# Kernel tuning notes

Measured on AMD Instinct MI355X. Metric: run time of the kernel, lower is better.

## Reference

```python
import jax, jax.numpy as jnp
import numpy as np

N = 100000      # nodes
E = 1600000     # edges (avg degree 16)
IN, HID, OUT = 128, 64, 64


def setup_inputs() -> dict:
    key = jax.random.key(0)
    ks = jax.random.split(key, 8)
    s = 0.05
    return {
        "x": jax.random.normal(ks[0], (N, IN), jnp.float32),
        "edge_index": jax.random.randint(ks[1], (2, E), 0, N, dtype=jnp.int32),
        "W1": jax.random.normal(ks[2], (IN, HID), jnp.float32) * s,
        "b1": jnp.zeros((HID,), jnp.float32),
        "W2": jax.random.normal(ks[3], (HID, HID), jnp.float32) * s,
        "b2": jnp.zeros((HID,), jnp.float32),
        "W3": jax.random.normal(ks[4], (HID, OUT), jnp.float32) * s,
        "b3": jnp.zeros((OUT,), jnp.float32),
    }


def reference(x, edge_index, W1, b1, W2, b2, W3, b3):
    src, dst = edge_index[0], edge_index[1]

    def gcn_conv(h, W, b):
        # GCNConv(normalize=False): dense linear, gather source features,
        # scatter-add into target nodes, add bias.
        m = (h @ W)[src]                                   # [E, F_out]
        return jax.ops.segment_sum(m, dst, num_segments=N) + b

    h = jax.nn.relu(gcn_conv(x, W1, b1))   # dropout: identity (eval mode)
    h = jax.nn.relu(gcn_conv(h, W2, b2))
    return jax.nn.sigmoid(gcn_conv(h, W3, b3))
```

## Files before the change

### kernel.cpp

```cpp
#include <hip/hip_runtime.h>


#define FOUT 64
#define NPB2 196
#define NBUCKET 511
#define CAP 4096
#define CHUNK 8192

__device__ __forceinline__ unsigned short f2bf(float f) {
    unsigned u = __float_as_uint(f);
    u += 0x7FFF + ((u >> 16) & 1);
    return (unsigned short)(u >> 16);
}
__device__ __forceinline__ float bflo(unsigned u) {
    return __uint_as_float(u << 16);
}
__device__ __forceinline__ float bfhi(unsigned u) {
    return __uint_as_float(u & 0xFFFF0000u);
}
__device__ __forceinline__ unsigned pack2(float lo, float hi) {
    return (unsigned)f2bf(lo) | ((unsigned)f2bf(hi) << 16);
}

template<int K, int INBF>
__global__ __launch_bounds__(256) void k_linear(
    const void* __restrict__ inv, const float* __restrict__ W,
    unsigned short* __restrict__ outbf, int n) {
    constexpr int XSTR = (K == 128) ? 132 : 68;
    __shared__ float4 sW4[K * 16];
    __shared__ float xs[64 * XSTR];

    const int t = threadIdx.x;
    const int base = blockIdx.x * 64;

    const float4* W4 = (const float4*)W;
#pragma unroll
    for (int i = 0; i < K * 16 / 256; ++i) sW4[t + i * 256] = W4[t + i * 256];

    if (INBF) {
        const unsigned short* in16 = (const unsigned short*)inv;
        constexpr int QPR = K / 8;
#pragma unroll
        for (int i = 0; i < 64 * QPR / 256; ++i) {
            int flat = t + i * 256;
            int row = flat / QPR;
            int q = flat % QPR;
            int rg = base + row;
            if (rg < n) {
                uint4 u = *(const uint4*)(in16 + (size_t)rg * K + q * 8);
                float* xp = &xs[row * XSTR + q * 8];
                float4 a, b;
                a.x = bflo(u.x); a.y = bfhi(u.x);
                a.z = bflo(u.y); a.w = bfhi(u.y);
                b.x = bflo(u.z); b.y = bfhi(u.z);
                b.z = bflo(u.w); b.w = bfhi(u.w);
                *(float4*)(xp) = a;
                *(float4*)(xp + 4) = b;
            }
        }
    } else {
        const float* in = (const float*)inv;
        constexpr int CPR = K / 4;
#pragma unroll
        for (int i = 0; i < 64 * CPR / 256; ++i) {
            int flat = t + i * 256;
            int row = flat / CPR;
            int c4 = flat % CPR;
            int rg = base + row;
            if (rg < n) {
                float4 v = *(const float4*)(in + (size_t)rg * K + c4 * 4);
                *(float4*)&xs[row * XSTR + c4 * 4] = v;
            }
        }
    }
    __syncthreads();

    const int fq = t & 15;
    const int slot = (t >> 4) & 3;
    const int wave = t >> 6;
    const int r0 = wave * 16 + slot * 4;

    float4 acc[4];
#pragma unroll
    for (int i = 0; i < 4; ++i) acc[i] = make_float4(0.f, 0.f, 0.f, 0.f);

#pragma unroll 8
    for (int k = 0; k < K; k += 4) {
        float4 w0 = sW4[(k + 0) * 16 + fq];
        float4 w1 = sW4[(k + 1) * 16 + fq];
        float4 w2 = sW4[(k + 2) * 16 + fq];
        float4 w3 = sW4[(k + 3) * 16 + fq];
#pragma unroll
        for (int i = 0; i < 4; ++i) {
            float4 xv = *(const float4*)&xs[(r0 + i) * XSTR + k];
            acc[i].x = fmaf(xv.x, w0.x, acc[i].x);
            acc[i].y = fmaf(xv.x, w0.y, acc[i].y);
            acc[i].z = fmaf(xv.x, w0.z, acc[i].z);
            acc[i].w = fmaf(xv.x, w0.w, acc[i].w);
            acc[i].x = fmaf(xv.y, w1.x, acc[i].x);
            acc[i].y = fmaf(xv.y, w1.y, acc[i].y);
            acc[i].z = fmaf(xv.y, w1.z, acc[i].z);
            acc[i].w = fmaf(xv.y, w1.w, acc[i].w);
            acc[i].x = fmaf(xv.z, w2.x, acc[i].x);
            acc[i].y = fmaf(xv.z, w2.y, acc[i].y);
            acc[i].z = fmaf(xv.z, w2.z, acc[i].z);
            acc[i].w = fmaf(xv.z, w2.w, acc[i].w);
            acc[i].x = fmaf(xv.w, w3.x, acc[i].x);
            acc[i].y = fmaf(xv.w, w3.y, acc[i].y);
            acc[i].z = fmaf(xv.w, w3.z, acc[i].z);
            acc[i].w = fmaf(xv.w, w3.w, acc[i].w);
        }
    }

#pragma unroll
    for (int i = 0; i < 4; ++i) {
        int rg = base + r0 + i;
        if (rg < n) {
            ushort4 us;
            us.x = f2bf(acc[i].x); us.y = f2bf(acc[i].y);
            us.z = f2bf(acc[i].z); us.w = f2bf(acc[i].w);
            *(ushort4*)(outbf + (size_t)rg * FOUT + fq * 4) = us;
        }
    }
}

__global__ __launch_bounds__(512) void k_init(int* __restrict__ gcursor) {
    gcursor[threadIdx.x] = threadIdx.x * CAP;
}

__global__ __launch_bounds__(256) void k_bin(
    const int* __restrict__ src, const int* __restrict__ dst,
    int* __restrict__ gcursor, int* __restrict__ bins, int ne) {
    __shared__ int cnt[NBUCKET];
    __shared__ int gbase[NBUCKET];

    const int t = threadIdx.x;
    const int cbeg = blockIdx.x * CHUNK;
    const int cend = min(cbeg + CHUNK, ne);

    for (int i = t; i < NBUCKET; i += 256) cnt[i] = 0;
    __syncthreads();

    for (int e = cbeg + t; e < cend; e += 256)
        atomicAdd(&cnt[dst[e] / NPB2], 1);
    __syncthreads();

    for (int i = t; i < NBUCKET; i += 256) {
        int c = cnt[i];
        gbase[i] = (c > 0) ? atomicAdd(&gcursor[i], c) : 0;
    }
    __syncthreads();
    for (int i = t; i < NBUCKET; i += 256) cnt[i] = 0;
    __syncthreads();

    for (int e = cbeg + t; e < cend; e += 256) {
        int d = dst[e];
        int b = d / NPB2;
        int dl = d - b * NPB2;
        int lpos = atomicAdd(&cnt[b], 1);
        int gpos = gbase[b] + lpos;
        if (gpos < (b + 1) * CAP)
            bins[gpos] = src[e] | (dl << 17);
    }
}

__global__ __launch_bounds__(512) void k_bscan(
    const int* __restrict__ gcursor, int* __restrict__ bucket_base) {
    __shared__ int s[512];
    const int t = threadIdx.x;
    int c = 0;
    if (t < NBUCKET) c = min(gcursor[t] - t * CAP, CAP);
    s[t] = c;
    __syncthreads();
    for (int ofs = 1; ofs < 512; ofs <<= 1) {
        int v = (t >= ofs) ? s[t - ofs] : 0;
        __syncthreads();
        s[t] += v;
        __syncthreads();
    }
    if (t < NBUCKET) bucket_base[t] = s[t] - c;
}

__global__ __launch_bounds__(256) void k_csr(
    const int* __restrict__ gcursor, const int* __restrict__ bins,
    const int* __restrict__ bucket_base, int* __restrict__ row_ofs,
    int* __restrict__ csr_src, int n) {
    __shared__ int recs[CAP];
    __shared__ int cnt[NPB2];
    __shared__ int cur[NPB2];
    __shared__ int sscan[256];

    const int t = threadIdx.x;
    const int b = blockIdx.x;
    const int c = min(gcursor[b] - b * CAP, CAP);
    const int baseg = bucket_base[b];

    for (int i = t; i < c; i += 256) recs[i] = bins[b * CAP + i];
    for (int i = t; i < NPB2; i += 256) cnt[i] = 0;
    __syncthreads();

    for (int i = t; i < c; i += 256)
        atomicAdd(&cnt[((unsigned)recs[i]) >> 17], 1);
    __syncthreads();

    int v = (t < NPB2) ? cnt[t] : 0;
    sscan[t] = v;
    __syncthreads();
    for (int o = 1; o < 256; o <<= 1) {
        int u = (t >= o) ? sscan[t - o] : 0;
        __syncthreads();
        sscan[t] += u;
        __syncthreads();
    }
    if (t < NPB2) {
        cur[t] = sscan[t] - v;
        int node = b * NPB2 + t;
        if (node <= n) row_ofs[node] = baseg + sscan[t] - v;
    }
    __syncthreads();

    for (int i = t; i < c; i += 256) {
        unsigned r = (unsigned)recs[i];
        int dl = r >> 17;
        int p = atomicAdd(&cur[dl], 1);
        csr_src[baseg + p] = (int)(r & 0x1FFFF);
    }
}

template<int ACT, int OUTBF>
__global__ __launch_bounds__(256) void k_agg(
    const int* __restrict__ row_ofs, const int* __restrict__ csr_src,
    const uint4* __restrict__ msg4, const float* __restrict__ bias,
    void* __restrict__ outv, int n) {
    const int node = blockIdx.x * 4 + (threadIdx.x >> 6);
    if (node >= n) return;
    const int lane = threadIdx.x & 63;
    const int e8 = lane >> 3;
    const int fo = lane & 7;
    const int beg = row_ofs[node];
    const int end = row_ofs[node + 1];

    float a0 = 0.f, a1 = 0.f, a2 = 0.f, a3 = 0.f;
    float a4 = 0.f, a5 = 0.f, a6 = 0.f, a7 = 0.f;

    for (int j = beg + e8; j < end; j += 8) {
        int s = csr_src[j];
        uint4 v = msg4[(size_t)s * 8 + fo];
        a0 += bflo(v.x); a1 += bfhi(v.x);
        a2 += bflo(v.y); a3 += bfhi(v.y);
        a4 += bflo(v.z); a5 += bfhi(v.z);
        a6 += bflo(v.w); a7 += bfhi(v.w);
    }

#pragma unroll
    for (int m = 8; m < 64; m <<= 1) {
        a0 += __shfl_xor(a0, m); a1 += __shfl_xor(a1, m);
        a2 += __shfl_xor(a2, m); a3 += __shfl_xor(a3, m);
        a4 += __shfl_xor(a4, m); a5 += __shfl_xor(a5, m);
        a6 += __shfl_xor(a6, m); a7 += __shfl_xor(a7, m);
    }

    if (e8 == 0) {
        const float4 b0 = *(const float4*)(bias + fo * 8);
        const float4 b1 = *(const float4*)(bias + fo * 8 + 4);
        float v0 = a0 + b0.x, v1 = a1 + b0.y, v2 = a2 + b0.z, v3 = a3 + b0.w;
        float v4 = a4 + b1.x, v5 = a5 + b1.y, v6 = a6 + b1.z, v7 = a7 + b1.w;
        if (ACT == 0) {
            v0 = fmaxf(v0, 0.f); v1 = fmaxf(v1, 0.f);
            v2 = fmaxf(v2, 0.f); v3 = fmaxf(v3, 0.f);
            v4 = fmaxf(v4, 0.f); v5 = fmaxf(v5, 0.f);
            v6 = fmaxf(v6, 0.f); v7 = fmaxf(v7, 0.f);
        } else {
            v0 = 1.f / (1.f + __expf(-v0)); v1 = 1.f / (1.f + __expf(-v1));
            v2 = 1.f / (1.f + __expf(-v2)); v3 = 1.f / (1.f + __expf(-v3));
            v4 = 1.f / (1.f + __expf(-v4)); v5 = 1.f / (1.f + __expf(-v5));
            v6 = 1.f / (1.f + __expf(-v6)); v7 = 1.f / (1.f + __expf(-v7));
        }
        if (OUTBF) {
            uint4 u;
            u.x = pack2(v0, v1); u.y = pack2(v2, v3);
            u.z = pack2(v4, v5); u.w = pack2(v6, v7);
            *(uint4*)((unsigned short*)outv + (size_t)node * FOUT + fo * 8) = u;
        } else {
            float* op = (float*)outv + (size_t)node * FOUT + fo * 8;
            *(float4*)op = make_float4(v0, v1, v2, v3);
            *(float4*)(op + 4) = make_float4(v4, v5, v6, v7);
        }
    }
}

extern "C" void kernel_launch(void* const* d_in, const int* in_sizes, int n_in,
                              void* d_out, int out_size, void* d_ws, size_t ws_size,
                              hipStream_t stream) {
    const float* x  = (const float*)d_in[0];
    const int*   ei = (const int*)d_in[1];
    const float* W1 = (const float*)d_in[2];
    const float* b1 = (const float*)d_in[3];
    const float* W2 = (const float*)d_in[4];
    const float* b2 = (const float*)d_in[5];
    const float* W3 = (const float*)d_in[6];
    const float* b3 = (const float*)d_in[7];
    float* out = (float*)d_out;

    const int n  = in_sizes[0] / 128;
    const int ne = in_sizes[1] / 2;
    const int* src = ei;
    const int* dst = ei + ne;

    const size_t feat_elems = (size_t)n * FOUT;

    unsigned short* msg16 = (unsigned short*)d_ws;
    unsigned short* B16   = msg16 + feat_elems;
    int*   bins     = (int*)(B16 + feat_elems);
    int*   gcursor  = bins + (size_t)NBUCKET * CAP;
    int*   bucket_base = gcursor + 512;
    int*   row_ofs  = bucket_base + 512;
    int*   csr_src  = row_ofs + n + 1;

    const int gLin = (n + 63) / 64;
    const int gBin = (ne + CHUNK - 1) / CHUNK;
    const int gAgg = (n + 3) / 4;

    k_init<<<1, NBUCKET, 0, stream>>>(gcursor);
    k_bin<<<gBin, 256, 0, stream>>>(src, dst, gcursor, bins, ne);
    k_bscan<<<1, 512, 0, stream>>>(gcursor, bucket_base);
    k_csr<<<NBUCKET, 256, 0, stream>>>(gcursor, bins, bucket_base, row_ofs, csr_src, n);

    k_linear<128, 0><<<gLin, 256, 0, stream>>>(x, W1, msg16, n);
    k_agg<0, 1><<<gAgg, 256, 0, stream>>>(row_ofs, csr_src, (const uint4*)msg16, b1, B16, n);
    k_linear<64, 1><<<gLin, 256, 0, stream>>>(B16, W2, msg16, n);
    k_agg<0, 1><<<gAgg, 256, 0, stream>>>(row_ofs, csr_src, (const uint4*)msg16, b2, B16, n);
    k_linear<64, 1><<<gLin, 256, 0, stream>>>(B16, W3, msg16, n);
    k_agg<1, 0><<<gAgg, 256, 0, stream>>>(row_ofs, csr_src, (const uint4*)msg16, b3, out, n);
}
```

Before: 356.7 us.

## Fold bucket scan into CSR kernel and aggregate four nodes per wave

Drops the separate single-block bucket prefix-scan launch; each CSR block now computes its own base offset by summing the counts of all preceding buckets with a block reduction. The aggregation kernel changes from one node per 64-lane wave to four nodes per wave, with 16 lanes per node handling two edges at a time. This needs a single shuffle step instead of three and reduces idle lanes on low-degree nodes. The cost is redundant prefix work in every CSR block and fewer edges in flight per node, so high-degree nodes take longer.

```diff
diff --git a/kernel.cpp b/kernel.cpp
--- a/kernel.cpp
+++ b/kernel.cpp
@@ -164,36 +164,30 @@
     }
 }
 
-__global__ __launch_bounds__(512) void k_bscan(
-    const int* __restrict__ gcursor, int* __restrict__ bucket_base) {
-    __shared__ int s[512];
-    const int t = threadIdx.x;
-    int c = 0;
-    if (t < NBUCKET) c = min(gcursor[t] - t * CAP, CAP);
-    s[t] = c;
-    __syncthreads();
-    for (int ofs = 1; ofs < 512; ofs <<= 1) {
-        int v = (t >= ofs) ? s[t - ofs] : 0;
-        __syncthreads();
-        s[t] += v;
-        __syncthreads();
-    }
-    if (t < NBUCKET) bucket_base[t] = s[t] - c;
-}
-
 __global__ __launch_bounds__(256) void k_csr(
     const int* __restrict__ gcursor, const int* __restrict__ bins,
-    const int* __restrict__ bucket_base, int* __restrict__ row_ofs,
-    int* __restrict__ csr_src, int n) {
+    int* __restrict__ row_ofs, int* __restrict__ csr_src, int n) {
     __shared__ int recs[CAP];
     __shared__ int cnt[NPB2];
     __shared__ int cur[NPB2];
     __shared__ int sscan[256];
+    __shared__ int spart[256];
 
     const int t = threadIdx.x;
     const int b = blockIdx.x;
     const int c = min(gcursor[b] - b * CAP, CAP);
-    const int baseg = bucket_base[b];
+
+    int part = 0;
+    for (int i = t; i < b; i += 256)
+        part += min(gcursor[i] - i * CAP, CAP);
+    spart[t] = part;
+    __syncthreads();
+    for (int o = 128; o > 0; o >>= 1) {
+        if (t < o) spart[t] += spart[t + o];
+        __syncthreads();
+    }
+    const int baseg = spart[0];
+    __syncthreads();
 
     for (int i = t; i < c; i += 256) recs[i] = bins[b * CAP + i];
     for (int i = t; i < NPB2; i += 256) cnt[i] = 0;
@@ -232,18 +226,23 @@
     const int* __restrict__ row_ofs, const int* __restrict__ csr_src,
     const uint4* __restrict__ msg4, const float* __restrict__ bias,
     void* __restrict__ outv, int n) {
-    const int node = blockIdx.x * 4 + (threadIdx.x >> 6);
-    if (node >= n) return;
+    const int wave = threadIdx.x >> 6;
     const int lane = threadIdx.x & 63;
-    const int e8 = lane >> 3;
+    const int nsub = lane >> 4;
+    const int e2 = (lane >> 3) & 1;
     const int fo = lane & 7;
-    const int beg = row_ofs[node];
-    const int end = row_ofs[node + 1];
+    const int node = (blockIdx.x * 4 + wave) * 4 + nsub;
+
+    int beg = 0, end = 0;
+    if (node < n) {
+        beg = row_ofs[node];
+        end = row_ofs[node + 1];
+    }
 
     float a0 = 0.f, a1 = 0.f, a2 = 0.f, a3 = 0.f;
     float a4 = 0.f, a5 = 0.f, a6 = 0.f, a7 = 0.f;
 
-    for (int j = beg + e8; j < end; j += 8) {
+    for (int j = beg + e2; j < end; j += 2) {
         int s = csr_src[j];
         uint4 v = msg4[(size_t)s * 8 + fo];
         a0 += bflo(v.x); a1 += bfhi(v.x);
@@ -252,15 +251,12 @@
         a6 += bflo(v.w); a7 += bfhi(v.w);
     }
 
-#pragma unroll
-    for (int m = 8; m < 64; m <<= 1) {
-        a0 += __shfl_xor(a0, m); a1 += __shfl_xor(a1, m);
-        a2 += __shfl_xor(a2, m); a3 += __shfl_xor(a3, m);
-        a4 += __shfl_xor(a4, m); a5 += __shfl_xor(a5, m);
-        a6 += __shfl_xor(a6, m); a7 += __shfl_xor(a7, m);
-    }
-
-    if (e8 == 0) {
+    a0 += __shfl_xor(a0, 8); a1 += __shfl_xor(a1, 8);
+    a2 += __shfl_xor(a2, 8); a3 += __shfl_xor(a3, 8);
+    a4 += __shfl_xor(a4, 8); a5 += __shfl_xor(a5, 8);
+    a6 += __shfl_xor(a6, 8); a7 += __shfl_xor(a7, 8);
+
+    if (e2 == 0 && node < n) {
         const float4 b0 = *(const float4*)(bias + fo * 8);
         const float4 b1 = *(const float4*)(bias + fo * 8 + 4);
         float v0 = a0 + b0.x, v1 = a1 + b0.y, v2 = a2 + b0.z, v3 = a3 + b0.w;
@@ -313,18 +309,16 @@
     unsigned short* B16   = msg16 + feat_elems;
     int*   bins     = (int*)(B16 + feat_elems);
     int*   gcursor  = bins + (size_t)NBUCKET * CAP;
-    int*   bucket_base = gcursor + 512;
-    int*   row_ofs  = bucket_base + 512;
+    int*   row_ofs  = gcursor + 512;
     int*   csr_src  = row_ofs + n + 1;
 
     const int gLin = (n + 63) / 64;
     const int gBin = (ne + CHUNK - 1) / CHUNK;
-    const int gAgg = (n + 3) / 4;
+    const int gAgg = (n + 15) / 16;
 
     k_init<<<1, NBUCKET, 0, stream>>>(gcursor);
     k_bin<<<gBin, 256, 0, stream>>>(src, dst, gcursor, bins, ne);
-    k_bscan<<<1, 512, 0, stream>>>(gcursor, bucket_base);
-    k_csr<<<NBUCKET, 256, 0, stream>>>(gcursor, bins, bucket_base, row_ofs, csr_src, n);
+    k_csr<<<NBUCKET, 256, 0, stream>>>(gcursor, bins, row_ofs, csr_src, n);
 
     k_linear<128, 0><<<gLin, 256, 0, stream>>>(x, W1, msg16, n);
     k_agg<0, 1><<<gAgg, 256, 0, stream>>>(row_ofs, csr_src, (const uint4*)msg16, b1, B16, n);
```

New measurement: 330.1 us. -7.5%, faster.
